# Optimization experiments

Hardware: AMD Instinct MI355X
Metric: run time of the kernel (lower is better)

Reference implementation:

```python
import jax, jax.numpy as jnp
import numpy as np

B, H, N, D, W = 2, 12, 2048, 128, 64  # batch, heads, seq, head_dim (1536/12), nnz per row


def setup_inputs() -> dict:
    key = jax.random.key(0)
    kq, kk, kv, kc = jax.random.split(key, 4)
    q = jax.random.normal(kq, (B, H, N, D), jnp.float32)
    k = jax.random.normal(kk, (B, H, N, D), jnp.float32)
    v = jax.random.normal(kv, (B, H, N, D), jnp.float32)
    # CSR-style sparse attention topology: each query row attends to W columns,
    # column indices sorted within each row (as Sputnik requires).
    col_ids = jnp.sort(jax.random.randint(kc, (N, W), 0, N, dtype=jnp.int32), axis=-1)
    return {"q": q, "k": k, "v": v, "col_ids": col_ids}


def reference(q, k, v, col_ids):
    # SDDMM: scores only at sparse positions -> [B, H, N, W]
    scale = 1.0 / jnp.sqrt(jnp.float32(q.shape[-1]))
    kg = k[:, :, col_ids]  # gather K rows per sparse column: [B, H, N, W, D]
    scores = jnp.einsum('bhnd,bhnwd->bhnw', q, kg) * scale
    # Row-wise sparse softmax (fixed W nnz per row -> dense softmax over last axis)
    probs = jax.nn.softmax(scores, axis=-1)
    # SPMM: sparse probs @ V -> [B, H, N, D]
    vg = v[:, :, col_ids]  # [B, H, N, W, D]
    return jnp.einsum('bhnw,bhnwd->bhnd', probs, vg)
```

## Files before the change

kernel.cpp:

```cpp
#include <hip/hip_runtime.h>
#include <hip/hip_bf16.h>
#include <hip/hip_fp16.h>

constexpr int Bc = 2;
constexpr int Hc = 12;
constexpr int Nc = 2048;
constexpr int Dc = 128;
constexpr int Wc = 64;
constexpr float SCALE = 0.08838834764831845f;
constexpr int ELEMS = Bc * Hc * Nc * Dc;

typedef _Float16 h2v __attribute__((ext_vector_type(2)));
typedef float    f32x4 __attribute__((ext_vector_type(4)));

__device__ __forceinline__ unsigned packh2(float a, float b) {
    const __half2 h = __floats2half2_rn(a, b);
    return __builtin_bit_cast(unsigned, h);
}

__device__ __forceinline__ __half2 bc2(unsigned u) {
    return __builtin_bit_cast(__half2, u);
}

__device__ __forceinline__ float dot2h(unsigned kp, unsigned qp, float acc) {
#if __has_builtin(__builtin_amdgcn_fdot2)
    return __builtin_amdgcn_fdot2(__builtin_bit_cast(h2v, kp),
                                  __builtin_bit_cast(h2v, qp), acc, false);
#else
    const float2 kf = __half22float2(bc2(kp));
    const float2 qf = __half22float2(bc2(qp));
    return acc + kf.x * qf.x + kf.y * qf.y;
#endif
}

__global__ __launch_bounds__(256) void cvt_kernel(
    const float* __restrict__ k,
    const float* __restrict__ v,
    unsigned* __restrict__ kh,
    unsigned* __restrict__ vh)
{
    const int i = blockIdx.x * 256 + threadIdx.x;
    const float4 kk = ((const float4*)k)[i];
    const float4 vv = ((const float4*)v)[i];
    uint2 ko, vo;
    ko.x = packh2(kk.x, kk.y);  ko.y = packh2(kk.z, kk.w);
    vo.x = packh2(vv.x, vv.y);  vo.y = packh2(vv.z, vv.w);
    ((uint2*)kh)[i] = ko;
    ((uint2*)vh)[i] = vo;
}

__global__ __launch_bounds__(256) void sca_wave_kernel(
    const float* __restrict__ q,
    const unsigned short* __restrict__ kh,
    const unsigned short* __restrict__ vh,
    const int*   __restrict__ col_ids,
    float*       __restrict__ out)
{
    const int t    = threadIdx.x;
    const int wv   = t >> 6;
    const int lane = t & 63;

    const int i    = blockIdx.x;
    const int xcd  = i & 7;
    const int slot = i >> 3;
    const int hg   = slot % 3;
    const int nb   = slot / 3;
    const int bh   = xcd + 8 * hg;
    const int n    = nb * 4 + wv;
    const int row  = bh * Nc + n;

    const int c_own = col_ids[n * Wc + lane];

    const float*          qrow  = q  + (size_t)row * Dc;
    const unsigned short* kbase = kh + (size_t)bh * Nc * Dc;
    const unsigned short* vbase = vh + (size_t)bh * Nc * Dc;

    const int p8 = lane & 7;
    const int o8 = lane >> 3;

    const f32x4* q4 = (const f32x4*)qrow;
    const f32x4 qa0 = __builtin_nontemporal_load(&q4[2 * p8]);
    const f32x4 qa1 = __builtin_nontemporal_load(&q4[2 * p8 + 1]);
    const f32x4 qb0 = __builtin_nontemporal_load(&q4[16 + 2 * p8]);
    const f32x4 qb1 = __builtin_nontemporal_load(&q4[16 + 2 * p8 + 1]);
    unsigned qp[8];
    qp[0] = packh2(qa0[0], qa0[1]);  qp[1] = packh2(qa0[2], qa0[3]);
    qp[2] = packh2(qa1[0], qa1[1]);  qp[3] = packh2(qa1[2], qa1[3]);
    qp[4] = packh2(qb0[0], qb0[1]);  qp[5] = packh2(qb0[2], qb0[3]);
    qp[6] = packh2(qb1[0], qb1[1]);  qp[7] = packh2(qb1[2], qb1[3]);

    int cc[8];
#pragma unroll
    for (int P = 0; P < 8; ++P) cc[P] = __shfl(c_own, 8 * P + o8);

    float s = 0.0f;
    __half2 ah[8];
#pragma unroll
    for (int d = 0; d < 8; ++d) ah[d] = __floats2half2_rn(0.0f, 0.0f);

#pragma unroll
    for (int P = 0; P < 8; ++P) {
        const uint4* kr = (const uint4*)(kbase + (size_t)cc[P] * Dc);
        const uint4* vr = (const uint4*)(vbase + (size_t)cc[P] * Dc);
        const uint4 k0 = kr[p8];
        const uint4 k1 = kr[8 + p8];
        const uint4 w0 = vr[p8];
        const uint4 w1 = vr[8 + p8];
        float a0 = 0.0f, a1 = 0.0f;
        a0 = dot2h(k0.x, qp[0], a0);
        a0 = dot2h(k0.y, qp[1], a0);
        a0 = dot2h(k0.z, qp[2], a0);
        a0 = dot2h(k0.w, qp[3], a0);
        a1 = dot2h(k1.x, qp[4], a1);
        a1 = dot2h(k1.y, qp[5], a1);
        a1 = dot2h(k1.z, qp[6], a1);
        a1 = dot2h(k1.w, qp[7], a1);
        float acc = a0 + a1;
        acc += __shfl_xor(acc, 1);
        acc += __shfl_xor(acc, 2);
        acc += __shfl_xor(acc, 4);
        const float e = __expf(acc * SCALE);
        s += e;
        const __half2 eh = __floats2half2_rn(e, e);
        ah[0] = __hfma2(bc2(w0.x), eh, ah[0]);
        ah[1] = __hfma2(bc2(w0.y), eh, ah[1]);
        ah[2] = __hfma2(bc2(w0.z), eh, ah[2]);
        ah[3] = __hfma2(bc2(w0.w), eh, ah[3]);
        ah[4] = __hfma2(bc2(w1.x), eh, ah[4]);
        ah[5] = __hfma2(bc2(w1.y), eh, ah[5]);
        ah[6] = __hfma2(bc2(w1.z), eh, ah[6]);
        ah[7] = __hfma2(bc2(w1.w), eh, ah[7]);
    }

#pragma unroll
    for (int off = 8; off < 64; off <<= 1) s += __shfl_xor(s, off);
    const float inv = 1.0f / s;

    float f[16];
#pragma unroll
    for (int d = 0; d < 8; ++d) {
        const float2 u = __half22float2(ah[d]);
        f[2 * d]     = u.x;
        f[2 * d + 1] = u.y;
    }
#pragma unroll
    for (int off = 8; off < 64; off <<= 1) {
#pragma unroll
        for (int d = 0; d < 16; ++d) f[d] += __shfl_xor(f[d], off);
    }

    if (lane < 8) {
#pragma unroll
        for (int d = 0; d < 16; ++d) f[d] *= inv;
        f32x4* orow = (f32x4*)(out + (size_t)row * Dc);
        f32x4 o0; o0[0] = f[0];  o0[1] = f[1];  o0[2] = f[2];  o0[3] = f[3];
        f32x4 o1; o1[0] = f[4];  o1[1] = f[5];  o1[2] = f[6];  o1[3] = f[7];
        f32x4 o2; o2[0] = f[8];  o2[1] = f[9];  o2[2] = f[10]; o2[3] = f[11];
        f32x4 o3; o3[0] = f[12]; o3[1] = f[13]; o3[2] = f[14]; o3[3] = f[15];
        __builtin_nontemporal_store(o0, &orow[2 * p8]);
        __builtin_nontemporal_store(o1, &orow[2 * p8 + 1]);
        __builtin_nontemporal_store(o2, &orow[16 + 2 * p8]);
        __builtin_nontemporal_store(o3, &orow[17 + 2 * p8]);
    }
}

__global__ __launch_bounds__(256) void sca_kernel(
    const float* __restrict__ q,
    const float* __restrict__ k,
    const float* __restrict__ v,
    const int*   __restrict__ col_ids,
    float*       __restrict__ out)
{
    const int bid = blockIdx.x;
    const int n   = bid & (Nc - 1);
    const int bh  = bid >> 11;
    const int t   = threadIdx.x;

    __shared__ int   s_cols[Wc];
    __shared__ float s_scores[Wc];
    __shared__ float s_probs[Wc];
    __shared__ float s_red[8 * Dc];

    if (t < Wc) s_cols[t] = col_ids[n * Wc + t];

    const float* qrow  = q + ((size_t)bh * Nc + n) * Dc;
    const float* kbase = k + (size_t)bh * Nc * Dc;
    const float* vbase = v + (size_t)bh * Nc * Dc;

    __syncthreads();
    {
        const int w = t >> 2;
        const int p = t & 3;
        const int c = s_cols[w];
        const float4* krow = (const float4*)(kbase + (size_t)c * Dc);
        const float4* q4   = (const float4*)qrow;
        float acc = 0.0f;
#pragma unroll
        for (int i = 0; i < 8; ++i) {
            const float4 kk = krow[p + 4 * i];
            const float4 qq = q4[p + 4 * i];
            acc += kk.x * qq.x + kk.y * qq.y + kk.z * qq.z + kk.w * qq.w;
        }
        acc += __shfl_xor(acc, 1);
        acc += __shfl_xor(acc, 2);
        if (p == 0) s_scores[w] = acc * SCALE;
    }
    __syncthreads();
    if (t < 64) {
        const float sv = s_scores[t];
        float m = sv;
#pragma unroll
        for (int off = 32; off > 0; off >>= 1) m = fmaxf(m, __shfl_xor(m, off));
        const float e = __expf(sv - m);
        float l = e;
#pragma unroll
        for (int off = 32; off > 0; off >>= 1) l += __shfl_xor(l, off);
        s_probs[t] = e / l;
    }
    __syncthreads();
    {
        const int j = t & 31;
        const int g = t >> 5;
        float4 acc = make_float4(0.f, 0.f, 0.f, 0.f);
#pragma unroll
        for (int i = 0; i < 8; ++i) {
            const int w  = g * 8 + i;
            const float pr = s_probs[w];
            const int   c  = s_cols[w];
            const float4 vv = ((const float4*)(vbase + (size_t)c * Dc))[j];
            acc.x += pr * vv.x;
            acc.y += pr * vv.y;
            acc.z += pr * vv.z;
            acc.w += pr * vv.w;
        }
        ((float4*)s_red)[g * 32 + j] = acc;
    }
    __syncthreads();
    if (t < Dc) {
        float sv = 0.0f;
#pragma unroll
        for (int g = 0; g < 8; ++g) sv += s_red[g * Dc + t];
        out[((size_t)bh * Nc + n) * Dc + t] = sv;
    }
}

extern "C" void kernel_launch(void* const* d_in, const int* in_sizes, int n_in,
                              void* d_out, int out_size, void* d_ws, size_t ws_size,
                              hipStream_t stream) {
    const float* q       = (const float*)d_in[0];
    const float* k       = (const float*)d_in[1];
    const float* v       = (const float*)d_in[2];
    const int*   col_ids = (const int*)  d_in[3];
    float*       out     = (float*)d_out;

    const int n_rows = Bc * Hc * Nc;
    const size_t need = (size_t)2 * ELEMS * sizeof(unsigned short);

    if (ws_size >= need) {
        unsigned* khp = (unsigned*)d_ws;
        unsigned* vhp = khp + ELEMS / 2;
        cvt_kernel<<<dim3(ELEMS / 4 / 256), dim3(256), 0, stream>>>(k, v, khp, vhp);
        sca_wave_kernel<<<dim3(n_rows / 4), dim3(256), 0, stream>>>(
            q, (const unsigned short*)khp, (const unsigned short*)vhp, col_ids, out);
    } else {
        sca_kernel<<<dim3(n_rows), dim3(256), 0, stream>>>(q, k, v, col_ids, out);
    }
}
```

Measured before the change: 182.0 us.

## Issue all K/V gather loads upfront via inline asm with staged vmcnt waits

```diff
diff --git a/kernel.cpp b/kernel.cpp
--- a/kernel.cpp
+++ b/kernel.cpp
@@ -10,8 +10,9 @@
 constexpr float SCALE = 0.08838834764831845f;
 constexpr int ELEMS = Bc * Hc * Nc * Dc;
 
-typedef _Float16 h2v __attribute__((ext_vector_type(2)));
-typedef float    f32x4 __attribute__((ext_vector_type(4)));
+typedef _Float16     h2v   __attribute__((ext_vector_type(2)));
+typedef float        f32x4 __attribute__((ext_vector_type(4)));
+typedef unsigned int u32x4 __attribute__((ext_vector_type(4)));
 
 __device__ __forceinline__ unsigned packh2(float a, float b) {
     const __half2 h = __floats2half2_rn(a, b);
@@ -49,7 +50,7 @@
     ((uint2*)vh)[i] = vo;
 }
 
-__global__ __launch_bounds__(256) void sca_wave_kernel(
+__global__ __launch_bounds__(256, 2) void sca_wave_kernel(
     const float* __restrict__ q,
     const unsigned short* __restrict__ kh,
     const unsigned short* __restrict__ vh,
@@ -78,59 +79,105 @@
     const int p8 = lane & 7;
     const int o8 = lane >> 3;
 
-    const f32x4* q4 = (const f32x4*)qrow;
-    const f32x4 qa0 = __builtin_nontemporal_load(&q4[2 * p8]);
-    const f32x4 qa1 = __builtin_nontemporal_load(&q4[2 * p8 + 1]);
-    const f32x4 qb0 = __builtin_nontemporal_load(&q4[16 + 2 * p8]);
-    const f32x4 qb1 = __builtin_nontemporal_load(&q4[16 + 2 * p8 + 1]);
+    int cc[8];
+#pragma unroll
+    for (int P = 0; P < 8; ++P) cc[P] = __shfl(c_own, 8 * P + o8);
+
+    u32x4 qra0, qra1, qrb0, qrb1;
+    {
+        const u32x4* qa_ = (const u32x4*)qrow + 2 * p8;
+        const u32x4* qb_ = (const u32x4*)qrow + 16 + 2 * p8;
+        asm volatile("global_load_dwordx4 %0, %2, off sc1\n\t"
+                     "global_load_dwordx4 %1, %2, off offset:16 sc1"
+                     : "=&v"(qra0), "=&v"(qra1) : "v"(qa_));
+        asm volatile("global_load_dwordx4 %0, %2, off sc1\n\t"
+                     "global_load_dwordx4 %1, %2, off offset:16 sc1"
+                     : "=&v"(qrb0), "=&v"(qrb1) : "v"(qb_));
+    }
+
+    u32x4 K0[8], K1[8], V0[8], V1[8];
+#define ISSUE_PASS(P)                                                         \
+    do {                                                                      \
+        const u32x4* ka_ = (const u32x4*)(kbase + (size_t)cc[P] * Dc) + p8;   \
+        const u32x4* va_ = (const u32x4*)(vbase + (size_t)cc[P] * Dc) + p8;   \
+        asm volatile("global_load_dwordx4 %0, %4, off sc1\n\t"                \
+                     "global_load_dwordx4 %1, %4, off offset:128 sc1\n\t"     \
+                     "global_load_dwordx4 %2, %5, off sc1\n\t"                \
+                     "global_load_dwordx4 %3, %5, off offset:128 sc1"         \
+                     : "=&v"(K0[P]), "=&v"(K1[P]),                            \
+                       "=&v"(V0[P]), "=&v"(V1[P])                             \
+                     : "v"(ka_), "v"(va_));                                   \
+    } while (0)
+
+    ISSUE_PASS(0); ISSUE_PASS(1); ISSUE_PASS(2); ISSUE_PASS(3);
+    ISSUE_PASS(4); ISSUE_PASS(5); ISSUE_PASS(6); ISSUE_PASS(7);
+#undef ISSUE_PASS
+
+    asm volatile("s_waitcnt vmcnt(32)"
+                 : "+v"(qra0), "+v"(qra1), "+v"(qrb0), "+v"(qrb1));
+#if __has_builtin(__builtin_amdgcn_sched_barrier)
+    __builtin_amdgcn_sched_barrier(0);
+#endif
+    const f32x4 qa0 = __builtin_bit_cast(f32x4, qra0);
+    const f32x4 qa1 = __builtin_bit_cast(f32x4, qra1);
+    const f32x4 qb0 = __builtin_bit_cast(f32x4, qrb0);
+    const f32x4 qb1 = __builtin_bit_cast(f32x4, qrb1);
     unsigned qp[8];
     qp[0] = packh2(qa0[0], qa0[1]);  qp[1] = packh2(qa0[2], qa0[3]);
     qp[2] = packh2(qa1[0], qa1[1]);  qp[3] = packh2(qa1[2], qa1[3]);
     qp[4] = packh2(qb0[0], qb0[1]);  qp[5] = packh2(qb0[2], qb0[3]);
     qp[6] = packh2(qb1[0], qb1[1]);  qp[7] = packh2(qb1[2], qb1[3]);
 
-    int cc[8];
-#pragma unroll
-    for (int P = 0; P < 8; ++P) cc[P] = __shfl(c_own, 8 * P + o8);
-
     float s = 0.0f;
     __half2 ah[8];
 #pragma unroll
     for (int d = 0; d < 8; ++d) ah[d] = __floats2half2_rn(0.0f, 0.0f);
 
-#pragma unroll
-    for (int P = 0; P < 8; ++P) {
-        const uint4* kr = (const uint4*)(kbase + (size_t)cc[P] * Dc);
-        const uint4* vr = (const uint4*)(vbase + (size_t)cc[P] * Dc);
-        const uint4 k0 = kr[p8];
-        const uint4 k1 = kr[8 + p8];
-        const uint4 w0 = vr[p8];
-        const uint4 w1 = vr[8 + p8];
-        float a0 = 0.0f, a1 = 0.0f;
-        a0 = dot2h(k0.x, qp[0], a0);
-        a0 = dot2h(k0.y, qp[1], a0);
-        a0 = dot2h(k0.z, qp[2], a0);
-        a0 = dot2h(k0.w, qp[3], a0);
-        a1 = dot2h(k1.x, qp[4], a1);
-        a1 = dot2h(k1.y, qp[5], a1);
-        a1 = dot2h(k1.z, qp[6], a1);
-        a1 = dot2h(k1.w, qp[7], a1);
-        float acc = a0 + a1;
-        acc += __shfl_xor(acc, 1);
-        acc += __shfl_xor(acc, 2);
-        acc += __shfl_xor(acc, 4);
-        const float e = __expf(acc * SCALE);
-        s += e;
-        const __half2 eh = __floats2half2_rn(e, e);
-        ah[0] = __hfma2(bc2(w0.x), eh, ah[0]);
-        ah[1] = __hfma2(bc2(w0.y), eh, ah[1]);
-        ah[2] = __hfma2(bc2(w0.z), eh, ah[2]);
-        ah[3] = __hfma2(bc2(w0.w), eh, ah[3]);
-        ah[4] = __hfma2(bc2(w1.x), eh, ah[4]);
-        ah[5] = __hfma2(bc2(w1.y), eh, ah[5]);
-        ah[6] = __hfma2(bc2(w1.z), eh, ah[6]);
-        ah[7] = __hfma2(bc2(w1.w), eh, ah[7]);
-    }
+#define WAIT_PASS(P, CNT)                                                     \
+    do {                                                                      \
+        asm volatile("s_waitcnt vmcnt(" #CNT ")"                              \
+                     : "+v"(K0[P]), "+v"(K1[P]), "+v"(V0[P]), "+v"(V1[P]));   \
+        __builtin_amdgcn_sched_barrier(0);                                    \
+    } while (0)
+
+#define COMPUTE_PASS(P)                                                       \
+    do {                                                                      \
+        float a0 = 0.0f, a1 = 0.0f;                                           \
+        a0 = dot2h(K0[P][0], qp[0], a0);                                      \
+        a0 = dot2h(K0[P][1], qp[1], a0);                                      \
+        a0 = dot2h(K0[P][2], qp[2], a0);                                      \
+        a0 = dot2h(K0[P][3], qp[3], a0);                                      \
+        a1 = dot2h(K1[P][0], qp[4], a1);                                      \
+        a1 = dot2h(K1[P][1], qp[5], a1);                                      \
+        a1 = dot2h(K1[P][2], qp[6], a1);                                      \
+        a1 = dot2h(K1[P][3], qp[7], a1);                                      \
+        float acc = a0 + a1;                                                  \
+        acc += __shfl_xor(acc, 1);                                            \
+        acc += __shfl_xor(acc, 2);                                            \
+        acc += __shfl_xor(acc, 4);                 \
+        const float e = __expf(acc * SCALE);                  \
+        s += e;                                                               \
+        const __half2 eh = __floats2half2_rn(e, e);                           \
+        ah[0] = __hfma2(bc2(V0[P][0]), eh, ah[0]);                            \
+        ah[1] = __hfma2(bc2(V0[P][1]), eh, ah[1]);                            \
+        ah[2] = __hfma2(bc2(V0[P][2]), eh, ah[2]);                            \
+        ah[3] = __hfma2(bc2(V0[P][3]), eh, ah[3]);                            \
+        ah[4] = __hfma2(bc2(V1[P][0]), eh, ah[4]);                            \
+        ah[5] = __hfma2(bc2(V1[P][1]), eh, ah[5]);                            \
+        ah[6] = __hfma2(bc2(V1[P][2]), eh, ah[6]);                            \
+        ah[7] = __hfma2(bc2(V1[P][3]), eh, ah[7]);                            \
+    } while (0)
+
+    WAIT_PASS(0, 28); COMPUTE_PASS(0);
+    WAIT_PASS(1, 24); COMPUTE_PASS(1);
+    WAIT_PASS(2, 20); COMPUTE_PASS(2);
+    WAIT_PASS(3, 16); COMPUTE_PASS(3);
+    WAIT_PASS(4, 12); COMPUTE_PASS(4);
+    WAIT_PASS(5, 8);  COMPUTE_PASS(5);
+    WAIT_PASS(6, 4);  COMPUTE_PASS(6);
+    WAIT_PASS(7, 0);  COMPUTE_PASS(7);
+#undef WAIT_PASS
+#undef COMPUTE_PASS
 
 #pragma unroll
     for (int off = 8; off < 64; off <<= 1) s += __shfl_xor(s, off);
```

New measurement: 178.9 us. No clear change (-1.7%).
